# Optimization experiments

Hardware: AMD Instinct MI355X
Metric: run time of the kernel (lower is better)

Reference implementation:

```python
import jax, jax.numpy as jnp
import numpy as np

# Dimensions (see shape_source): 28 indices per sample, values in [0, 8)
NX, NY, DIM, VOCAB = 2048, 2048, 28, 8
INTRA, INTER = 1.0, 2.0  # intra_class_distance, inter_class_distance
NCLS = 3
# index -> class id, derived from set_list = [[3,4,5,6],[0,1,2],[7]]
LUT = jnp.array([1, 1, 1, 0, 0, 0, 0, 2], dtype=jnp.int32)


def setup_inputs() -> dict:
    key = jax.random.key(0)
    k1, k2 = jax.random.split(key)
    return {
        "set_r": jax.random.randint(k1, (NX, DIM), 0, VOCAB, dtype=jnp.int32),
        "set_t": jax.random.randint(k2, (NY, DIM), 0, VOCAB, dtype=jnp.int32),
        "sigma": jnp.ones((), dtype=jnp.float32),
    }


def reference(set_r, set_t, sigma):
    # Per-position distance rule (from vector_distance, since set_list covers
    # every index exactly once):
    #   r == t                -> 0
    #   class(r) == class(t)  -> INTRA
    #   otherwise             -> INTER
    # sum over positions = INTRA*(cls_eq_cnt - eq_cnt) + INTER*(DIM - cls_eq_cnt)
    # Counts of matching positions are computed as one-hot GEMMs to avoid a
    # [NX, NY, DIM] intermediate.
    oh_r = jax.nn.one_hot(set_r, VOCAB, dtype=jnp.float32)       # [NX, DIM, V]
    oh_t = jax.nn.one_hot(set_t, VOCAB, dtype=jnp.float32)       # [NY, DIM, V]
    eq_cnt = jnp.einsum('idv,jdv->ij', oh_r, oh_t)               # [NX, NY]
    ch_r = jax.nn.one_hot(LUT[set_r], NCLS, dtype=jnp.float32)   # [NX, DIM, C]
    ch_t = jax.nn.one_hot(LUT[set_t], NCLS, dtype=jnp.float32)   # [NY, DIM, C]
    cls_cnt = jnp.einsum('idc,jdc->ij', ch_r, ch_t)              # [NX, NY]
    dist = (INTRA * (cls_cnt - eq_cnt) + INTER * (DIM - cls_cnt)) / DIM
    # Gaussain_kernel: exp(-d^2 / (2*sigma^2))
    return jnp.exp(-(dist ** 2) / (2.0 * sigma ** 2))
```

## Files before the change

kernel.cpp:

```cpp
#include <hip/hip_runtime.h>
#include <stdint.h>

#define NXD 2048
#define NYD 2048
#define DIMD 28
#define CLS_TABLE 0x20000111u

__device__ __forceinline__ void pack_row(const int* __restrict__ src,
                                         uint32_t* __restrict__ w ) {
    int vals[DIMD];
    const int4* s4 = (const int4*)src;
#pragma unroll
    for (int q = 0; q < 7; ++q) {
        int4 t = s4[q];
        vals[4*q+0] = t.x; vals[4*q+1] = t.y;
        vals[4*q+2] = t.z; vals[4*q+3] = t.w;
    }
    unsigned long long e0=0, e1=0, e2=0, e3=0, c0=0, c1=0;
#pragma unroll
    for (int d = 0; d < DIMD; ++d) {
        const int v = vals[d];
        const unsigned long long eb = 1ull << (((d*8) & 63) + v);
        if      (d < 8)  e0 |= eb;
        else if (d < 16) e1 |= eb;
        else if (d < 24) e2 |= eb;
        else             e3 |= eb;
        const int c = (CLS_TABLE >> (4*v)) & 0xF;
        if      (d*3 + 2 < 64) c0 |= 1ull << (d*3 + c);
        else if (d*3 >= 64)    c1 |= 1ull << (d*3 - 64 + c);
        else {
            const unsigned long long b = 1ull << c;
            c0 |= (b & 1ull) << 63;
            c1 |= b >> 1;
        }
    }
    w[0]=(uint32_t)e0; w[1]=(uint32_t)(e0>>32);
    w[2]=(uint32_t)e1; w[3]=(uint32_t)(e1>>32);
    w[4]=(uint32_t)e2; w[5]=(uint32_t)(e2>>32);
    w[6]=(uint32_t)e3;
    w[7]=(uint32_t)c0; w[8]=(uint32_t)(c0>>32);
    w[9]=(uint32_t)c1;
    w[10]=0u; w[11]=0u;
}

__global__ __launch_bounds__(256) void setdist_kernel(
    const int* __restrict__ set_r, const int* __restrict__ set_t,
    const float* __restrict__ sigma_p, float* __restrict__ out)
{
    __shared__ uint32_t t_pk[256][12];
    __shared__ uint32_t r_pk[32][12];

    const int tid = threadIdx.x;
    const int i0 = blockIdx.y * 32;
    const int j0 = blockIdx.x * 256;

    {
        uint32_t w[12];
        pack_row(set_t + (size_t)(j0 + tid) * DIMD, w);
        uint4* dst = (uint4*)t_pk[tid];
        dst[0] = make_uint4(w[0], w[1], w[2], w[3]);
        dst[1] = make_uint4(w[4], w[5], w[6], w[7]);
        dst[2] = make_uint4(w[8], w[9], 0u, 0u);
    }
    if (tid < 32) {
        uint32_t w[12];
        pack_row(set_r + (size_t)(i0 + tid) * DIMD, w);
        uint4* dst = (uint4*)r_pk[tid];
        dst[0] = make_uint4(w[0], w[1], w[2], w[3]);
        dst[1] = make_uint4(w[4], w[5], w[6], w[7]);
        dst[2] = make_uint4(w[8], w[9], 0u, 0u);
    }

    const float sg = sigma_p[0];
    const float k = 1.0f / (2.0f * sg * sg * (float)(DIMD * DIMD));

    __syncthreads();

    const int lane = tid & 63;
    const int wave = tid >> 6;

    uint4 T[4][3];
#pragma unroll
    for (int s = 0; s < 4; ++s) {
        const uint4* tp = (const uint4*)t_pk[lane + 64*s];
        T[s][0] = tp[0]; T[s][1] = tp[1]; T[s][2] = tp[2];
    }

    float* obase = out + (size_t)(i0 + wave * 8) * NYD + j0 + lane;

#pragma unroll
    for (int ii = 0; ii < 8; ++ii) {
        const uint4* rp = (const uint4*)r_pk[wave * 8 + ii];
        const uint4 R0 = rp[0], R1 = rp[1], R2 = rp[2];
#pragma unroll
        for (int s = 0; s < 4; ++s) {
            const int sum =
                __popc(R0.x & T[s][0].x) + __popc(R0.y & T[s][0].y) +
                __popc(R0.z & T[s][0].z) + __popc(R0.w & T[s][0].w) +
                __popc(R1.x & T[s][1].x) + __popc(R1.y & T[s][1].y) +
                __popc(R1.z & T[s][1].z) + __popc(R1.w & T[s][1].w) +
                __popc(R2.x & T[s][2].x) + __popc(R2.y & T[s][2].y);
            const float c = (float)(56 - sum);
            obase[(size_t)ii * NYD + 64 * s] = __expf(-c * c * k);
        }
    }
}

extern "C" void kernel_launch(void* const* d_in, const int* in_sizes, int n_in,
                              void* d_out, int out_size, void* d_ws, size_t ws_size,
                              hipStream_t stream) {
    const int*   set_r = (const int*)d_in[0];
    const int*   set_t = (const int*)d_in[1];
    const float* sigma = (const float*)d_in[2];
    float*       out   = (float*)d_out;

    setdist_kernel<<<dim3(NYD / 256, NXD / 32), dim3(256), 0, stream>>>(
        set_r, set_t, sigma, out);
}
```

Measured before the change: 67.28 us.

## Split packing into a separate pre-pass kernel and read packed rows from workspace

```diff
diff --git a/kernel.cpp b/kernel.cpp
--- a/kernel.cpp
+++ b/kernel.cpp
@@ -43,55 +43,55 @@
     w[10]=0u; w[11]=0u;
 }
 
-__global__ __launch_bounds__(256) void setdist_kernel(
+__global__ __launch_bounds__(256) void pack_all(
     const int* __restrict__ set_r, const int* __restrict__ set_t,
-    const float* __restrict__ sigma_p, float* __restrict__ out)
+    uint4* __restrict__ ws)
 {
-    __shared__ uint32_t t_pk[256][12];
-    __shared__ uint32_t r_pk[32][12];
+    const int idx = blockIdx.x * 256 + threadIdx.x;
+    const bool is_t = (idx < NYD);
+    const int row = is_t ? idx : idx - NYD;
+    const int* src = is_t ? (set_t + (size_t)row * DIMD)
+                          : (set_r + (size_t)row * DIMD);
+    uint32_t w[12];
+    pack_row(src, w);
+    uint4* base = ws + (is_t ? 0 : 3 * NYD);
+    base[0 * NYD + row] = make_uint4(w[0], w[1], w[2], w[3]);
+    base[1 * NYD + row] = make_uint4(w[4], w[5], w[6], w[7]);
+    base[2 * NYD + row] = make_uint4(w[8], w[9], 0u, 0u);
+}
 
-    const int tid = threadIdx.x;
-    const int i0 = blockIdx.y * 32;
+__global__ __launch_bounds__(256, 4) void dist_kernel(
+    const uint4* __restrict__ ws, const float* __restrict__ sigma_p,
+    float* __restrict__ out)
+{
+    const int tid  = threadIdx.x;
+    const int lane = tid & 63;
+    const int wave = tid >> 6;
+    const int i0 = blockIdx.y * 16;
     const int j0 = blockIdx.x * 256;
 
-    {
-        uint32_t w[12];
-        pack_row(set_t + (size_t)(j0 + tid) * DIMD, w);
-        uint4* dst = (uint4*)t_pk[tid];
-        dst[0] = make_uint4(w[0], w[1], w[2], w[3]);
-        dst[1] = make_uint4(w[4], w[5], w[6], w[7]);
-        dst[2] = make_uint4(w[8], w[9], 0u, 0u);
-    }
-    if (tid < 32) {
-        uint32_t w[12];
-        pack_row(set_r + (size_t)(i0 + tid) * DIMD, w);
-        uint4* dst = (uint4*)r_pk[tid];
-        dst[0] = make_uint4(w[0], w[1], w[2], w[3]);
-        dst[1] = make_uint4(w[4], w[5], w[6], w[7]);
-        dst[2] = make_uint4(w[8], w[9], 0u, 0u);
+    const uint4* t4 = ws;
+    const uint4* r4 = ws + 3 * NYD;
+
+    uint4 T[4][3];
+#pragma unroll
+    for (int s = 0; s < 4; ++s) {
+        const int j = j0 + lane + 64 * s;
+#pragma unroll
+        for (int q = 0; q < 3; ++q) T[s][q] = t4[q * NYD + j];
     }
 
     const float sg = sigma_p[0];
     const float k = 1.0f / (2.0f * sg * sg * (float)(DIMD * DIMD));
 
-    __syncthreads();
-
-    const int lane = tid & 63;
-    const int wave = tid >> 6;
-
-    uint4 T[4][3];
-#pragma unroll
-    for (int s = 0; s < 4; ++s) {
-        const uint4* tp = (const uint4*)t_pk[lane + 64*s];
-        T[s][0] = tp[0]; T[s][1] = tp[1]; T[s][2] = tp[2];
-    }
-
-    float* obase = out + (size_t)(i0 + wave * 8) * NYD + j0 + lane;
+    const int irow = i0 + wave * 4;
+    float* obase = out + (size_t)irow * NYD + j0 + lane;
 
 #pragma unroll
-    for (int ii = 0; ii < 8; ++ii) {
-        const uint4* rp = (const uint4*)r_pk[wave * 8 + ii];
-        const uint4 R0 = rp[0], R1 = rp[1], R2 = rp[2];
+    for (int ii = 0; ii < 4; ++ii) {
+        const uint4 R0 = r4[0 * NXD + irow + ii];
+        const uint4 R1 = r4[1 * NXD + irow + ii];
+        const uint4 R2 = r4[2 * NXD + irow + ii];
 #pragma unroll
         for (int s = 0; s < 4; ++s) {
             const int sum =
@@ -113,7 +113,10 @@
     const int*   set_t = (const int*)d_in[1];
     const float* sigma = (const float*)d_in[2];
     float*       out   = (float*)d_out;
+    uint4*       ws    = (uint4*)d_ws;
 
-    setdist_kernel<<<dim3(NYD / 256, NXD / 32), dim3(256), 0, stream>>>(
-        set_r, set_t, sigma, out);
+    pack_all<<<dim3(4096 / 256), dim3(256), 0, stream>>>(set_r, set_t, ws);
+
+    dist_kernel<<<dim3(NYD / 256, NXD / 16), dim3(256), 0, stream>>>(
+        ws, sigma, out);
 }
```

New measurement: 70.02 us. +4.1%, slower.
